# Performance work log

Hardware: AMD Instinct MI355X
Metric: run time of the kernel (lower is better)

## Reference

```python
import jax, jax.numpy as jnp
import numpy as np

N = 100000   # nodes
E = 1600000  # edges
IN = 128
H = 128
OUT = 64
G = 512      # graphs in batch


def setup_inputs() -> dict:
    key = jax.random.key(0)
    ks = jax.random.split(key, 9)
    x = jax.random.normal(ks[0], (N, IN), jnp.float32)
    edge_index = jax.random.randint(ks[1], (2, E), 0, N, dtype=jnp.int64)
    batch = jnp.sort(jax.random.randint(ks[2], (N,), 0, G, dtype=jnp.int64))
    # Glorot-ish init for weights, zeros for biases (as in GCNConv / nn.Linear defaults)
    W1 = jax.random.normal(ks[3], (IN, H), jnp.float32) * (1.0 / np.sqrt(IN))
    b1 = jnp.zeros((H,), jnp.float32)
    W2 = jax.random.normal(ks[4], (H, H), jnp.float32) * (1.0 / np.sqrt(H))
    b2 = jnp.zeros((H,), jnp.float32)
    Wl = jax.random.normal(ks[5], (H, OUT), jnp.float32) * (1.0 / np.sqrt(H))
    bl = jnp.zeros((OUT,), jnp.float32)
    return dict(x=x, edge_index=edge_index, batch=batch,
                W1=W1, b1=b1, W2=W2, b2=b2, Wl=Wl, bl=bl)


def reference(x, edge_index, batch, W1, b1, W2, b2, Wl, bl):
    n = x.shape[0]
    loop = jnp.arange(n, dtype=edge_index.dtype)
    # GCNConv default: add self-loops, symmetric normalization D^-1/2 A D^-1/2
    src = jnp.concatenate([edge_index[0], loop])  # message sources
    dst = jnp.concatenate([edge_index[1], loop])  # aggregation targets
    deg = jax.ops.segment_sum(jnp.ones(src.shape[0], jnp.float32), dst, num_segments=n)
    dinv = jnp.where(deg > 0, jax.lax.rsqrt(deg), 0.0)
    norm = dinv[src] * dinv[dst]  # [E+N]

    def gcn_conv(h, W, b):
        h = h @ W                              # [N, H] linear transform first
        msg = h[src] * norm[:, None]           # gather + scale: [E+N, H]
        return jax.ops.segment_sum(msg, dst, num_segments=n) + b

    h = jax.nn.relu(gcn_conv(x, W1, b1))
    # dropout: eval mode (training=False) -> identity
    h = jax.nn.relu(gcn_conv(h, W2, b2))
    pooled = jax.ops.segment_sum(h, batch, num_segments=G)  # global_add_pool: [G, H]
    return pooled @ Wl + bl
```

## Files before the change

kernel.cpp:

```cpp
#include <hip/hip_runtime.h>
#include <hip/hip_bf16.h>

typedef unsigned short u16;
typedef unsigned int   u32;
typedef unsigned long long u64;
typedef long long      i64;
typedef __attribute__((ext_vector_type(8))) short short8;
typedef __attribute__((ext_vector_type(4))) float f32x4;

#define HD 128
#define OUTD 64
#define BSH 8
#define NBKT_MAX 512
#define PCHUNK 2048
#define GCUR_STRIDE 16

__device__ __forceinline__ float bf2f(u16 u){ union{u32 i; float f;} x; x.i=((u32)u)<<16; return x.f; }
__device__ __forceinline__ u16 f2bf(float f){ __hip_bfloat16 h=__float2bfloat16(f); return *reinterpret_cast<u16*>(&h); }
__device__ __forceinline__ float blo(u32 v){ union{u32 i; float f;} x; x.i=v<<16; return x.f; }
__device__ __forceinline__ float bhi(u32 v){ union{u32 i; float f;} x; x.i=v&0xffff0000u; return x.f; }

__device__ __forceinline__ short8 load8(const float* p){
  f32x4 lo = *reinterpret_cast<const f32x4*>(p);
  f32x4 hi = *reinterpret_cast<const f32x4*>(p + 4);
  short8 r;
  #pragma unroll
  for (int j=0;j<4;j++){ r[j]=(short)f2bf(lo[j]); r[4+j]=(short)f2bf(hi[j]); }
  return r;
}
__device__ __forceinline__ short8 load8(const u16* p){
  return *reinterpret_cast<const short8*>(p);
}

__device__ __forceinline__ int idx_at(const void* p, int i, int is32){
  return is32 ? ((const int*)p)[i] : (int)((const i64*)p)[i];
}

__global__ void k_zero_out(float* __restrict__ out, int n){
  int i = blockIdx.x*256 + threadIdx.x;
  if (i < n) out[i] = 0.f;
}

__global__ __launch_bounds__(256) void k_pack_w(
    const float* __restrict__ W1, u16* __restrict__ Wp1,
    const float* __restrict__ W2, u16* __restrict__ Wp2)
{
  const float* W  = blockIdx.x ? W2 : W1;
  u16*         Wp = blockIdx.x ? Wp2 : Wp1;
  for (int u = threadIdx.x; u < 2048; u += 256){
    int lane = u & 63, tc = u >> 6;
    int t = tc >> 2, c = tc & 3;
    int n = lane & 15, quad = lane >> 4;
    #pragma unroll
    for (int j=0;j<8;j++)
      Wp[(size_t)u*8 + j] = f2bf(W[(c*32 + quad*8 + j)*HD + t*16 + n]);
  }
}

__global__ __launch_bounds__(256) void k_init(
    const u32* __restrict__ ei, const u32* __restrict__ bw,
    int* __restrict__ flags, int* __restrict__ cnt, float* __restrict__ pooled,
    int npairs_e, int npairs_b, int N, int npool)
{
  int t = threadIdx.x;
  if (blockIdx.x == 0){
    if (t < 16) flags[t] = 0;
    __syncthreads();
    for (int i=t; i<npairs_e; i+=256) if (ei[2*i+1] != 0) atomicOr(&flags[0], 1);
    for (int i=t; i<npairs_b; i+=256) if (bw[2*i+1] != 0) atomicOr(&flags[1], 1);
  } else {
    int i = (blockIdx.x-1)*256 + t;
    if (i < N)     cnt[i] = 0;
    if (i < npool) pooled[i] = 0.f;
  }
}

__global__ __launch_bounds__(256) void k_sorted_count(
    const void* __restrict__ batch, const void* __restrict__ ei,
    int* __restrict__ flags, int* __restrict__ cnt, int n, int E, int NBc)
{
  if (blockIdx.x < NBc){
    int i = blockIdx.x*256 + threadIdx.x;
    if (i < n-1){
      int is32 = flags[1];
      if (idx_at(batch, i, is32) > idx_at(batch, i+1, is32)) atomicOr(&flags[2], 1);
    }
  } else {
    int e = (blockIdx.x - NBc)*256 + threadIdx.x;
    if (e < E){
      int d = idx_at(ei, E + e, flags[0]);
      atomicAdd(&cnt[d], 1);
    }
  }
}

__global__ void k_chunk_sums(const int* __restrict__ cnt, int* __restrict__ csum, int n){
  __shared__ int sd[256];
  int c=blockIdx.x, t=threadIdx.x;
  int base=c*1024+t*4, s=0;
  #pragma unroll
  for (int k=0;k<4;k++){ int i=base+k; if(i<n) s+=cnt[i]; }
  sd[t]=s; __syncthreads();
  for (int o=128;o>0;o>>=1){ if(t<o) sd[t]+=sd[t+o]; __syncthreads(); }
  if (t==0) csum[c]=sd[0];
}

__global__ void k_scan_chunks(const int* __restrict__ cnt, const int* __restrict__ csum,
                              int* __restrict__ row_ptr, int* __restrict__ gcur,
                              float* __restrict__ dinv, int n, int total, int nch){
  __shared__ int st[256];
  __shared__ int sd[256];
  int c=blockIdx.x, t=threadIdx.x;

  int s4=0;
  #pragma unroll
  for (int k=0;k<4;k++){ int i=t*4+k; if(i<nch) s4+=csum[i]; }
  st[t]=s4; __syncthreads();
  for (int o=1;o<256;o<<=1){ int x=(t>=o)?st[t-o]:0; __syncthreads(); st[t]+=x; __syncthreads(); }
  int cq=c>>2, cr=c&3;
  int cbase=(cq>0)?st[cq-1]:0;
  for (int k=0;k<cr;k++) cbase += csum[cq*4+k];

  int base=c*1024+t*4;
  int v[4], s=0;
  #pragma unroll
  for (int k=0;k<4;k++){ int i=base+k; v[k]=(i<n)?cnt[i]:0; s+=v[k]; }
  sd[t]=s; __syncthreads();
  for (int o=1;o<256;o<<=1){ int x=(t>=o)?sd[t-o]:0; __syncthreads(); sd[t]+=x; __syncthreads(); }
  int pre = cbase + ((t>0)?sd[t-1]:0);
  #pragma unroll
  for (int k=0;k<4;k++){
    int i=base+k;
    if (i<n){
      row_ptr[i]=pre;
      if ((i & ((1<<BSH)-1)) == 0) gcur[(i>>BSH)*GCUR_STRIDE] = pre;
      dinv[i]=rsqrtf((float)(v[k]+1));
      pre+=v[k];
    }
  }
  if (c==0 && t==0) row_ptr[n]=total;
}

__global__ __launch_bounds__(256) void k_part1(
    const void* __restrict__ ei, const int* __restrict__ flags,
    int* __restrict__ gcur, u32* __restrict__ pairs, int E)
{
  __shared__ int hist[NBKT_MAX];
  __shared__ int soff[NBKT_MAX];
  __shared__ int gb[NBKT_MAX];
  __shared__ int scant[256];
  __shared__ u32 stage[PCHUNK];
  __shared__ u16 sbkt[PCHUNK];

  int tid = threadIdx.x;
  hist[tid]=0; hist[tid+256]=0;
  __syncthreads();

  int base = blockIdx.x*PCHUNK;
  int is32 = flags[0];
  int d[PCHUNK/256], s[PCHUNK/256];
  #pragma unroll
  for (int k=0;k<PCHUNK/256;k++){
    int e = base + k*256 + tid;
    if (e < E){
      d[k]=idx_at(ei,E+e,is32); s[k]=idx_at(ei,e,is32);
      atomicAdd(&hist[d[k]>>BSH],1);
    } else d[k]=-1;
  }
  __syncthreads();

  int a0=hist[2*tid], a1=hist[2*tid+1];
  scant[tid]=a0+a1; __syncthreads();
  for (int o=1;o<256;o<<=1){ int x2=(tid>=o)?scant[tid-o]:0; __syncthreads(); scant[tid]+=x2; __syncthreads(); }
  int pre = (tid>0)?scant[tid-1]:0;
  soff[2*tid]=pre; soff[2*tid+1]=pre+a0;
  if (a0) gb[2*tid]   = atomicAdd(&gcur[(2*tid)*GCUR_STRIDE],   a0); else gb[2*tid]=0;
  if (a1) gb[2*tid+1] = atomicAdd(&gcur[(2*tid+1)*GCUR_STRIDE], a1); else gb[2*tid+1]=0;
  hist[2*tid]=0; hist[2*tid+1]=0;
  __syncthreads();

  #pragma unroll
  for (int k=0;k<PCHUNK/256;k++){
    if (d[k]>=0){
      int b = d[k]>>BSH;
      int loc = soff[b] + atomicAdd(&hist[b],1);
      stage[loc] = (u32)s[k] | ((u32)(d[k] & ((1<<BSH)-1)) << 24);
      sbkt[loc] = (u16)b;
    }
  }
  __syncthreads();

  int cnt_edges = E - base; if (cnt_edges > PCHUNK) cnt_edges = PCHUNK;
  for (int i=tid; i<cnt_edges; i+=256){
    int b = sbkt[i];
    pairs[(size_t)gb[b] + (i - soff[b])] = stage[i];
  }
}

template <typename TIN>
__global__ __launch_bounds__(256) void k_gemm_scale(
    const TIN* __restrict__ X, const u16* __restrict__ Wp,
    const float* __restrict__ dinv, u16* __restrict__ Gout, int nrows)
{
  int lane = threadIdx.x & 63;
  int wv   = threadIdx.x >> 6;
  int n    = lane & 15, quad = lane >> 4;

  const short8* wp = reinterpret_cast<const short8*>(Wp);
  short8 bf[8][4];
  #pragma unroll
  for (int t=0;t<8;t++)
    #pragma unroll
    for (int c=0;c<4;c++)
      bf[t][c] = wp[(t*4+c)*64 + lane];

  int ntiles = (nrows+15)>>4;
  int stride = gridDim.x*4;
  for (int tile = blockIdx.x*4 + wv; tile < ntiles; tile += stride){
    int ra = tile*16 + n;
    if (ra >= nrows) ra = nrows-1;
    const TIN* xp = X + (size_t)ra*HD + quad*8;
    short8 a[4];
    #pragma unroll
    for (int c=0;c<4;c++) a[c] = load8(xp + c*32);

    f32x4 acc[8];
    #pragma unroll
    for (int t=0;t<8;t++) acc[t] = (f32x4){0.f,0.f,0.f,0.f};
    #pragma unroll
    for (int c=0;c<4;c++)
      #pragma unroll
      for (int t=0;t<8;t++)
        acc[t] = __builtin_amdgcn_mfma_f32_16x16x32_bf16(a[c], bf[t][c], acc[t], 0,0,0);

    float dv[4]; int rw[4];
    #pragma unroll
    for (int r=0;r<4;r++){
      int row = tile*16 + quad*4 + r;
      rw[r]=row; dv[r]=(row<nrows)?dinv[row]:0.f;
    }
    #pragma unroll
    for (int t=0;t<8;t++)
      #pragma unroll
      for (int r=0;r<4;r++){
        int row = rw[r];
        if (row < nrows)
          Gout[(size_t)row*HD + t*16 + n] = f2bf(dv[r]*acc[t][r]);
      }
  }
}

__global__ __launch_bounds__(256) void k_part2(
    const u32* __restrict__ pairs, const int* __restrict__ row_ptr,
    int* __restrict__ colv, int N)
{
  __shared__ int lcur[1<<BSH];
  int b = blockIdx.x;
  int n0 = b<<BSH;
  int n1 = (b+1)<<BSH; if (n1 > N) n1 = N;
  int nn = n1 - n0;
  for (int i=threadIdx.x; i<nn; i+=256) lcur[i] = row_ptr[n0+i];
  __syncthreads();
  int lo = row_ptr[n0], hi = row_ptr[n1];
  for (int i = lo + threadIdx.x; i < hi; i += 256){
    u32 p = pairs[i];
    int s = (int)(p & 0xFFFFFFu), dl = (int)(p >> 24);
    int pos = atomicAdd(&lcur[dl], 1);
    colv[pos] = s;
  }
}

__global__ __launch_bounds__(256) void k_aggregate(
    const u16* __restrict__ g, const int* __restrict__ row_ptr,
    const int* __restrict__ colv, const float* __restrict__ dinv,
    const float* __restrict__ bias, u16* __restrict__ h, int n)
{
  int node = blockIdx.x*4 + (threadIdx.x>>6);
  if (node >= n) return;
  int lane = threadIdx.x & 63;
  int off = lane*2;

  u32 u = *reinterpret_cast<const u32*>(g + (size_t)node*HD + off);
  float ax = blo(u), ay = bhi(u);

  int s = row_ptr[node], e = row_ptr[node+1];
  int i = s;
  for (; i+16<=e; i+=16){
    u32 v[16];
    #pragma unroll
    for (int j=0;j<16;j++)
      v[j] = *reinterpret_cast<const u32*>(g+(size_t)colv[i+j]*HD+off);
    #pragma unroll
    for (int j=0;j<16;j++){ ax += blo(v[j]); ay += bhi(v[j]); }
  }
  if (i+8<=e){
    u32 v[8];
    #pragma unroll
    for (int j=0;j<8;j++)
      v[j] = *reinterpret_cast<const u32*>(g+(size_t)colv[i+j]*HD+off);
    #pragma unroll
    for (int j=0;j<8;j++){ ax += blo(v[j]); ay += bhi(v[j]); }
    i += 8;
  }
  if (i+4<=e){
    u32 v[4];
    #pragma unroll
    for (int j=0;j<4;j++)
      v[j] = *reinterpret_cast<const u32*>(g+(size_t)colv[i+j]*HD+off);
    #pragma unroll
    for (int j=0;j<4;j++){ ax += blo(v[j]); ay += bhi(v[j]); }
    i += 4;
  }
  for (; i<e; i++){
    u32 v=*reinterpret_cast<const u32*>(g+(size_t)colv[i]*HD+off);
    ax += blo(v); ay += bhi(v);
  }

  float dv = dinv[node];
  float rx = fmaxf(fmaf(dv, ax, bias[off]),   0.f);
  float ry = fmaxf(fmaf(dv, ay, bias[off+1]), 0.f);
  *reinterpret_cast<u32*>(h + (size_t)node*HD + off) = (u32)f2bf(rx) | ((u32)f2bf(ry)<<16);
}

__device__ __forceinline__ int lowerb(const void* a, int is32, int n, int key){
  int lo=0, hi=n;
  while (lo<hi){
    int mid=(lo+hi)>>1;
    if (idx_at(a, mid, is32) < key) lo=mid+1; else hi=mid;
  }
  return lo;
}

__global__ __launch_bounds__(256) void k_pool_final_sorted(
    const u16* __restrict__ h, const void* __restrict__ batch,
    const int* __restrict__ flags, const float* __restrict__ Wl,
    const float* __restrict__ bl, float* __restrict__ out, int n)
{
  if (flags[2]) return;
  __shared__ float sd[4][128];
  __shared__ float ps[128];
  __shared__ float racc[4][64];
  int gid = blockIdx.x, t = threadIdx.x;
  int w = t >> 6, lane = t & 63;
  int off = lane*2;
  int is32 = flags[1];
  int lo = lowerb(batch, is32, n, gid), hi = lowerb(batch, is32, n, gid+1);

  float ax = 0.f, ay = 0.f;
  int i = lo + w;
  for (; i + 12 < hi; i += 16){
    u32 v0 = *reinterpret_cast<const u32*>(h + (size_t)(i   )*HD + off);
    u32 v1 = *reinterpret_cast<const u32*>(h + (size_t)(i+ 4)*HD + off);
    u32 v2 = *reinterpret_cast<const u32*>(h + (size_t)(i+ 8)*HD + off);
    u32 v3 = *reinterpret_cast<const u32*>(h + (size_t)(i+12)*HD + off);
    ax += blo(v0)+blo(v1)+blo(v2)+blo(v3);
    ay += bhi(v0)+bhi(v1)+bhi(v2)+bhi(v3);
  }
  for (; i < hi; i += 4){
    u32 v = *reinterpret_cast<const u32*>(h + (size_t)i*HD + off);
    ax += blo(v); ay += bhi(v);
  }
  sd[w][off] = ax; sd[w][off+1] = ay;
  __syncthreads();
  if (t < 128) ps[t] = sd[0][t] + sd[1][t] + sd[2][t] + sd[3][t];
  __syncthreads();

  int o = t & 63, seg = t >> 6;
  float acc = 0.f;
  #pragma unroll
  for (int kk=0; kk<32; kk++){
    int k = seg*32 + kk;
    acc = fmaf(ps[k], Wl[k*OUTD + o], acc);
  }
  racc[seg][o] = acc;
  __syncthreads();
  if (t < 64)
    out[(size_t)gid*OUTD + t] = bl[t] + racc[0][t] + racc[1][t] + racc[2][t] + racc[3][t];
}

__global__ __launch_bounds__(256) void k_pool_atomic(
    const u16* __restrict__ h, const void* __restrict__ batch,
    const int* __restrict__ flags, float* __restrict__ pooled, int n)
{
  if (!flags[2]) return;
  int lane = threadIdx.x & 63;
  int off = lane*2;
  int is32 = flags[1];
  for (int node = blockIdx.x*4 + (threadIdx.x>>6); node < n; node += gridDim.x*4){
    int g = idx_at(batch, node, is32);
    u32 v = *reinterpret_cast<const u32*>(h + (size_t)node*HD + off);
    atomicAdd(&pooled[(size_t)g*HD + off],     blo(v));
    atomicAdd(&pooled[(size_t)g*HD + off + 1], bhi(v));
  }
}

__global__ void k_final(const float* __restrict__ pooled, const float* __restrict__ Wl,
                        const float* __restrict__ bl, const int* __restrict__ flags,
                        float* __restrict__ out){
  if (!flags[2]) return;
  int gid = blockIdx.x, t = threadIdx.x;
  float acc = bl[t];
  const float* p = pooled + gid*HD;
  #pragma unroll 8
  for (int k=0;k<HD;k++) acc = fmaf(p[k], Wl[k*OUTD + t], acc);
  out[gid*OUTD + t] = acc;
}

extern "C" void kernel_launch(void* const* d_in, const int* in_sizes, int n_in,
                              void* d_out, int out_size, void* d_ws, size_t ws_size,
                              hipStream_t stream)
{
  const float* x   = (const float*)d_in[0];
  const void*  ei  = d_in[1];
  const void*  bat = d_in[2];
  const float* W1  = (const float*)d_in[3];
  const float* b1  = (const float*)d_in[4];
  const float* W2  = (const float*)d_in[5];
  const float* b2  = (const float*)d_in[6];
  const float* Wl  = (const float*)d_in[7];
  const float* bl  = (const float*)d_in[8];
  float* out = (float*)d_out;

  int N = in_sizes[0] / HD;
  int E = in_sizes[1] / 2;
  int G = out_size / OUTD;
  int NCH = (N + 1023) / 1024;
  int nbins = (N + (1<<BSH) - 1) >> BSH;

  char* w = (char*)d_ws;
  size_t o = 0;
  auto alloc = [&](size_t b){ void* p = w + o; o += (b + 255) & ~(size_t)255; return p; };
  int*   cnt     = (int*)  alloc((size_t)N*4);
  int*   row_ptr = (int*)  alloc((size_t)(N+1)*4);
  int*   csum    = (int*)  alloc((size_t)NCH*4);
  int*   colv    = (int*)  alloc((size_t)E*4);
  u32*   pairs   = (u32*)  alloc((size_t)E*4);
  int*   gcur    = (int*)  alloc((size_t)NBKT_MAX*GCUR_STRIDE*4);
  float* dinv    = (float*)alloc((size_t)N*4);
  u16*   gbuf    = (u16*)  alloc((size_t)N*HD*2);
  u16*   hbuf    = (u16*)  alloc((size_t)N*HD*2);
  float* pooled  = (float*)alloc((size_t)G*HD*4);
  u16*   wp1     = (u16*)  alloc((size_t)HD*HD*2);
  u16*   wp2     = (u16*)  alloc((size_t)HD*HD*2);
  int*   flags   = (int*)  alloc(256);
  (void)n_in;

  if (o > ws_size || nbins > NBKT_MAX){
    k_zero_out<<<(out_size+255)/256, 256, 0, stream>>>(out, out_size);
    return;
  }

  int npairs_e = 4096; if (npairs_e > E) npairs_e = E;
  int npairs_b = 4096; if (npairs_b > N/2) npairs_b = N/2;
  int npool = G*HD;
  int nzb = (N+255)/256; { int pz = (npool+255)/256; if (pz > nzb) nzb = pz; }

  k_pack_w<<<2, 256, 0, stream>>>(W1, wp1, W2, wp2);
  k_init<<<1+nzb, 256, 0, stream>>>((const u32*)ei, (const u32*)bat, flags, cnt, pooled,
                                    npairs_e, npairs_b, N, npool);
  int NBc = (N+255)/256, NBe = (E+255)/256;
  k_sorted_count<<<NBc+NBe, 256, 0, stream>>>(bat, ei, flags, cnt, N, E, NBc);
  k_chunk_sums <<<NCH, 256, 0, stream>>>(cnt, csum, N);
  k_scan_chunks<<<NCH, 256, 0, stream>>>(cnt, csum, row_ptr, gcur, dinv, N, E, NCH);
  int npart = (E + PCHUNK - 1) / PCHUNK;
  k_part1<<<npart, 256, 0, stream>>>(ei, flags, gcur, pairs, E);
  k_gemm_scale<float><<<512, 256, 0, stream>>>(x, wp1, dinv, gbuf, N);
  k_part2<<<nbins, 256, 0, stream>>>(pairs, row_ptr, colv, N);
  k_aggregate <<<(N+3)/4, 256, 0, stream>>>(gbuf, row_ptr, colv, dinv, b1, hbuf, N);
  k_gemm_scale<u16><<<512, 256, 0, stream>>>(hbuf, wp2, dinv, gbuf, N);
  k_aggregate <<<(N+3)/4, 256, 0, stream>>>(gbuf, row_ptr, colv, dinv, b2, hbuf, N);
  k_pool_final_sorted<<<G, 256, 0, stream>>>(hbuf, bat, flags, Wl, bl, out, N);
  k_pool_atomic<<<1024, 256, 0, stream>>>(hbuf, bat, flags, pooled, N);
  k_final      <<<G, OUTD, 0, stream>>>(pooled, Wl, bl, flags, out);
}
```

Measured before the change: 422.8 us.

## Replace per-node global degree counting with bucket-level histograms and in-bucket CSR build

Per-node degree counting with global atomics, followed by two scan kernels, is replaced by a bucket-level histogram in shared memory that flushes only bucket counts to global memory, plus a single-block scan over buckets. Per-node counts, row_ptr and dinv are now computed inside the second partition kernel from each bucket's pairs using shared-memory atomics and a local scan. This removes 1.6M global atomics and two kernels. In exchange, part2 reads its pairs twice, and the first GEMM now has to wait for part2 because it needs dinv.

```diff
diff --git a/kernel.cpp b/kernel.cpp
--- a/kernel.cpp
+++ b/kernel.cpp
@@ -13,6 +13,7 @@
 #define BSH 8
 #define NBKT_MAX 512
 #define PCHUNK 2048
+#define EPB 4096
 #define GCUR_STRIDE 16
 
 __device__ __forceinline__ float bf2f(u16 u){ union{u32 i; float f;} x; x.i=((u32)u)<<16; return x.f; }
@@ -59,8 +60,8 @@
 
 __global__ __launch_bounds__(256) void k_init(
     const u32* __restrict__ ei, const u32* __restrict__ bw,
-    int* __restrict__ flags, int* __restrict__ cnt, float* __restrict__ pooled,
-    int npairs_e, int npairs_b, int N, int npool)
+    int* __restrict__ flags, int* __restrict__ bcntp, float* __restrict__ pooled,
+    int npairs_e, int npairs_b, int nbc, int npool)
 {
   int t = threadIdx.x;
   if (blockIdx.x == 0){
@@ -70,75 +71,56 @@
     for (int i=t; i<npairs_b; i+=256) if (bw[2*i+1] != 0) atomicOr(&flags[1], 1);
   } else {
     int i = (blockIdx.x-1)*256 + t;
-    if (i < N)     cnt[i] = 0;
+    if (i < nbc)   bcntp[i] = 0;
     if (i < npool) pooled[i] = 0.f;
   }
 }
 
-__global__ __launch_bounds__(256) void k_sorted_count(
+__global__ __launch_bounds__(256) void k_bucket_sorted(
     const void* __restrict__ batch, const void* __restrict__ ei,
-    int* __restrict__ flags, int* __restrict__ cnt, int n, int E, int NBc)
-{
+    int* __restrict__ flags, int* __restrict__ bcntp, int n, int E, int NBc)
+{
+  __shared__ int hist[NBKT_MAX];
+  int tid = threadIdx.x;
   if (blockIdx.x < NBc){
-    int i = blockIdx.x*256 + threadIdx.x;
+    int i = blockIdx.x*256 + tid;
     if (i < n-1){
       int is32 = flags[1];
       if (idx_at(batch, i, is32) > idx_at(batch, i+1, is32)) atomicOr(&flags[2], 1);
     }
-  } else {
-    int e = (blockIdx.x - NBc)*256 + threadIdx.x;
+    return;
+  }
+  hist[tid]=0; hist[tid+256]=0;
+  __syncthreads();
+  int base = (blockIdx.x - NBc)*EPB;
+  int is32 = flags[0];
+  #pragma unroll
+  for (int k=0;k<EPB/256;k++){
+    int e = base + k*256 + tid;
     if (e < E){
-      int d = idx_at(ei, E + e, flags[0]);
-      atomicAdd(&cnt[d], 1);
+      int d = idx_at(ei, E + e, is32);
+      atomicAdd(&hist[d>>BSH], 1);
     }
   }
-}
-
-__global__ void k_chunk_sums(const int* __restrict__ cnt, int* __restrict__ csum, int n){
-  __shared__ int sd[256];
-  int c=blockIdx.x, t=threadIdx.x;
-  int base=c*1024+t*4, s=0;
-  #pragma unroll
-  for (int k=0;k<4;k++){ int i=base+k; if(i<n) s+=cnt[i]; }
-  sd[t]=s; __syncthreads();
-  for (int o=128;o>0;o>>=1){ if(t<o) sd[t]+=sd[t+o]; __syncthreads(); }
-  if (t==0) csum[c]=sd[0];
-}
-
-__global__ void k_scan_chunks(const int* __restrict__ cnt, const int* __restrict__ csum,
-                              int* __restrict__ row_ptr, int* __restrict__ gcur,
-                              float* __restrict__ dinv, int n, int total, int nch){
-  __shared__ int st[256];
-  __shared__ int sd[256];
-  int c=blockIdx.x, t=threadIdx.x;
-
-  int s4=0;
-  #pragma unroll
-  for (int k=0;k<4;k++){ int i=t*4+k; if(i<nch) s4+=csum[i]; }
-  st[t]=s4; __syncthreads();
-  for (int o=1;o<256;o<<=1){ int x=(t>=o)?st[t-o]:0; __syncthreads(); st[t]+=x; __syncthreads(); }
-  int cq=c>>2, cr=c&3;
-  int cbase=(cq>0)?st[cq-1]:0;
-  for (int k=0;k<cr;k++) cbase += csum[cq*4+k];
-
-  int base=c*1024+t*4;
-  int v[4], s=0;
-  #pragma unroll
-  for (int k=0;k<4;k++){ int i=base+k; v[k]=(i<n)?cnt[i]:0; s+=v[k]; }
-  sd[t]=s; __syncthreads();
-  for (int o=1;o<256;o<<=1){ int x=(t>=o)?sd[t-o]:0; __syncthreads(); sd[t]+=x; __syncthreads(); }
-  int pre = cbase + ((t>0)?sd[t-1]:0);
-  #pragma unroll
-  for (int k=0;k<4;k++){
-    int i=base+k;
-    if (i<n){
-      row_ptr[i]=pre;
-      if ((i & ((1<<BSH)-1)) == 0) gcur[(i>>BSH)*GCUR_STRIDE] = pre;
-      dinv[i]=rsqrtf((float)(v[k]+1));
-      pre+=v[k];
-    }
-  }
-  if (c==0 && t==0) row_ptr[n]=total;
+  __syncthreads();
+  int a0=hist[2*tid], a1=hist[2*tid+1];
+  if (a0) atomicAdd(&bcntp[(2*tid)*GCUR_STRIDE],   a0);
+  if (a1) atomicAdd(&bcntp[(2*tid+1)*GCUR_STRIDE], a1);
+}
+
+__global__ __launch_bounds__(256) void k_bucket_scan(
+    const int* __restrict__ bcntp, int* __restrict__ gcur, int* __restrict__ bbase,
+    int* __restrict__ row_ptr, int N, int E)
+{
+  __shared__ int scant[256];
+  int t = threadIdx.x;
+  int a0 = bcntp[(2*t)*GCUR_STRIDE], a1 = bcntp[(2*t+1)*GCUR_STRIDE];
+  scant[t] = a0 + a1; __syncthreads();
+  for (int o=1;o<256;o<<=1){ int x=(t>=o)?scant[t-o]:0; __syncthreads(); scant[t]+=x; __syncthreads(); }
+  int pre = (t>0)?scant[t-1]:0;
+  gcur[(2*t)*GCUR_STRIDE]   = pre;      bbase[2*t]   = pre;
+  gcur[(2*t+1)*GCUR_STRIDE] = pre + a0; bbase[2*t+1] = pre + a0;
+  if (t == 255){ bbase[512] = pre + a0 + a1; row_ptr[N] = E; }
 }
 
 __global__ __launch_bounds__(256) void k_part1(
@@ -197,6 +179,40 @@
   }
 }
 
+__global__ __launch_bounds__(256) void k_part2ex(
+    const u32* __restrict__ pairs, const int* __restrict__ bbase,
+    int* __restrict__ row_ptr, float* __restrict__ dinv,
+    int* __restrict__ colv, int N)
+{
+  __shared__ int lcnt[1<<BSH];
+  __shared__ int sscan[256];
+  __shared__ int lcur[1<<BSH];
+  int b = blockIdx.x, t = threadIdx.x;
+  int n0 = b<<BSH;
+  int nn = N - n0; if (nn > 256) nn = 256;
+  int lo = bbase[b], hi = bbase[b+1];
+  lcnt[t] = 0; lcur[t] = lo;
+  __syncthreads();
+  for (int i = lo + t; i < hi; i += 256)
+    atomicAdd(&lcnt[pairs[i] >> 24], 1);
+  __syncthreads();
+  int c = lcnt[t];
+  sscan[t] = c; __syncthreads();
+  for (int o=1;o<256;o<<=1){ int x=(t>=o)?sscan[t-o]:0; __syncthreads(); sscan[t]+=x; __syncthreads(); }
+  int pre = (t>0)?sscan[t-1]:0;
+  if (t < nn){
+    row_ptr[n0+t] = lo + pre;
+    dinv[n0+t]    = rsqrtf((float)(c+1));
+    lcur[t]       = lo + pre;
+  }
+  __syncthreads();
+  for (int i = lo + t; i < hi; i += 256){
+    u32 p = pairs[i];
+    int pos = atomicAdd(&lcur[p>>24], 1);
+    if (pos >= lo && pos < hi) colv[pos] = (int)(p & 0xFFFFFFu);
+  }
+}
+
 template <typename TIN>
 __global__ __launch_bounds__(256) void k_gemm_scale(
     const TIN* __restrict__ X, const u16* __restrict__ Wp,
@@ -247,26 +263,6 @@
         if (row < nrows)
           Gout[(size_t)row*HD + t*16 + n] = f2bf(dv[r]*acc[t][r]);
       }
-  }
-}
-
-__global__ __launch_bounds__(256) void k_part2(
-    const u32* __restrict__ pairs, const int* __restrict__ row_ptr,
-    int* __restrict__ colv, int N)
-{
-  __shared__ int lcur[1<<BSH];
-  int b = blockIdx.x;
-  int n0 = b<<BSH;
-  int n1 = (b+1)<<BSH; if (n1 > N) n1 = N;
-  int nn = n1 - n0;
-  for (int i=threadIdx.x; i<nn; i+=256) lcur[i] = row_ptr[n0+i];
-  __syncthreads();
-  int lo = row_ptr[n0], hi = row_ptr[n1];
-  for (int i = lo + threadIdx.x; i < hi; i += 256){
-    u32 p = pairs[i];
-    int s = (int)(p & 0xFFFFFFu), dl = (int)(p >> 24);
-    int pos = atomicAdd(&lcur[dl], 1);
-    colv[pos] = s;
   }
 }
 
@@ -424,18 +420,17 @@
   int N = in_sizes[0] / HD;
   int E = in_sizes[1] / 2;
   int G = out_size / OUTD;
-  int NCH = (N + 1023) / 1024;
   int nbins = (N + (1<<BSH) - 1) >> BSH;
 
   char* w = (char*)d_ws;
   size_t o = 0;
   auto alloc = [&](size_t b){ void* p = w + o; o += (b + 255) & ~(size_t)255; return p; };
-  int*   cnt     = (int*)  alloc((size_t)N*4);
   int*   row_ptr = (int*)  alloc((size_t)(N+1)*4);
-  int*   csum    = (int*)  alloc((size_t)NCH*4);
   int*   colv    = (int*)  alloc((size_t)E*4);
   u32*   pairs   = (u32*)  alloc((size_t)E*4);
   int*   gcur    = (int*)  alloc((size_t)NBKT_MAX*GCUR_STRIDE*4);
+  int*   bcntp   = (int*)  alloc((size_t)NBKT_MAX*GCUR_STRIDE*4);
+  int*   bbase   = (int*)  alloc((size_t)(NBKT_MAX+1)*4);
   float* dinv    = (float*)alloc((size_t)N*4);
   u16*   gbuf    = (u16*)  alloc((size_t)N*HD*2);
   u16*   hbuf    = (u16*)  alloc((size_t)N*HD*2);
@@ -453,19 +448,19 @@
   int npairs_e = 4096; if (npairs_e > E) npairs_e = E;
   int npairs_b = 4096; if (npairs_b > N/2) npairs_b = N/2;
   int npool = G*HD;
-  int nzb = (N+255)/256; { int pz = (npool+255)/256; if (pz > nzb) nzb = pz; }
+  int nbc = NBKT_MAX*GCUR_STRIDE;
+  int nzb = (npool+255)/256; { int bz = (nbc+255)/256; if (bz > nzb) nzb = bz; }
 
   k_pack_w<<<2, 256, 0, stream>>>(W1, wp1, W2, wp2);
-  k_init<<<1+nzb, 256, 0, stream>>>((const u32*)ei, (const u32*)bat, flags, cnt, pooled,
-                                    npairs_e, npairs_b, N, npool);
-  int NBc = (N+255)/256, NBe = (E+255)/256;
-  k_sorted_count<<<NBc+NBe, 256, 0, stream>>>(bat, ei, flags, cnt, N, E, NBc);
-  k_chunk_sums <<<NCH, 256, 0, stream>>>(cnt, csum, N);
-  k_scan_chunks<<<NCH, 256, 0, stream>>>(cnt, csum, row_ptr, gcur, dinv, N, E, NCH);
+  k_init<<<1+nzb, 256, 0, stream>>>((const u32*)ei, (const u32*)bat, flags, bcntp, pooled,
+                                    npairs_e, npairs_b, nbc, npool);
+  int NBc = (N+255)/256, NPB = (E+EPB-1)/EPB;
+  k_bucket_sorted<<<NBc+NPB, 256, 0, stream>>>(bat, ei, flags, bcntp, N, E, NBc);
+  k_bucket_scan<<<1, 256, 0, stream>>>(bcntp, gcur, bbase, row_ptr, N, E);
   int npart = (E + PCHUNK - 1) / PCHUNK;
   k_part1<<<npart, 256, 0, stream>>>(ei, flags, gcur, pairs, E);
+  k_part2ex<<<nbins, 256, 0, stream>>>(pairs, bbase, row_ptr, dinv, colv, N);
   k_gemm_scale<float><<<512, 256, 0, stream>>>(x, wp1, dinv, gbuf, N);
-  k_part2<<<nbins, 256, 0, stream>>>(pairs, row_ptr, colv, N);
   k_aggregate <<<(N+3)/4, 256, 0, stream>>>(gbuf, row_ptr, colv, dinv, b1, hbuf, N);
   k_gemm_scale<u16><<<512, 256, 0, stream>>>(hbuf, wp2, dinv, gbuf, N);
   k_aggregate <<<(N+3)/4, 256, 0, stream>>>(gbuf, row_ptr, colv, dinv, b2, hbuf, N);
```

New measurement: 369.6 us. 12.6% less time.
